# Kernel tuning notes

Measured on AMD Instinct MI355X. Metric: run time of the kernel, lower is better.

## Reference

```python
import jax, jax.numpy as jnp
import numpy as np

B, D, T = 4, 1024, 512      # z: [B, input_dim, T]
V, CD = 32000, 4096          # codebook: [codebook_size, codebook_dim]
EPS = 1e-12                  # F.normalize default eps


def setup_inputs() -> dict:
    key = jax.random.key(0)
    k1, k2, k3, k4 = jax.random.split(key, 4)
    z = jax.random.normal(k1, (B, D, T), dtype=jnp.float32)
    codebook = jax.random.normal(k2, (V, CD), dtype=jnp.float32) * 0.02
    cb_w = jax.random.normal(k3, (D, CD), dtype=jnp.float32) * 0.02  # torch Linear weight [out,in]
    cb_b = jax.random.normal(k4, (D,), dtype=jnp.float32) * 0.02
    return {"z": z, "codebook": codebook, "cb_w": cb_w, "cb_b": cb_b}


def _l2norm(x):
    n = jnp.sqrt(jnp.sum(x * x, axis=1, keepdims=True))
    return x / jnp.maximum(n, EPS)


def reference(z, codebook, cb_w, cb_b):
    # stride == 1, use_cblinear == True -> z_e = z
    z_e = z                                              # [B, D, T]
    proj_cb = codebook @ cb_w.T + cb_b                    # [V, D] cb_proj(codebook)

    # decode_latents
    enc = jnp.transpose(z_e, (0, 2, 1)).reshape(-1, D)    # (B*T, D)
    enc_n = _l2norm(enc)
    cb_n = _l2norm(proj_cb)
    dist = (jnp.sum(enc_n * enc_n, axis=1, keepdims=True)
            - 2.0 * enc_n @ cb_n.T
            + jnp.sum(cb_n * cb_n, axis=1)[None, :])      # (B*T, V)
    indices = jnp.argmax(-dist, axis=1).reshape(B, T)     # argmin distance
    z_q = jnp.transpose(proj_cb[indices], (0, 2, 1))      # gather un-normalized codes -> [B, D, T]

    commitment_loss = jnp.mean((z_e - jax.lax.stop_gradient(z_q)) ** 2, axis=(1, 2))  # [B]
    codebook_loss = jnp.mean((z_q - jax.lax.stop_gradient(z_e)) ** 2, axis=(1, 2))    # [B]
    z_q_st = z_e + jax.lax.stop_gradient(z_q - z_e)       # straight-through
    return z_q_st, indices, commitment_loss, codebook_loss
```

## Files before the change

kernel.cpp:

```cpp
#include <hip/hip_runtime.h>
#include <hip/hip_bf16.h>
#include <math.h>

#define B_  4
#define D_  1024
#define T_  512
#define V_  32000
#define CD_ 4096
#define NR  (B_*T_)
#define VT2 (V_/256)

typedef __attribute__((ext_vector_type(8))) short short8v;
typedef __attribute__((ext_vector_type(4))) float f32x4;

#define MFMA16(a,b,c) __builtin_amdgcn_mfma_f32_16x16x32_bf16((a),(b),(c),0,0,0)

#define ASM_VMCNT8() asm volatile("s_waitcnt vmcnt(8)" ::: "memory")
#define ASM_VMCNT0() asm volatile("s_waitcnt vmcnt(0)" ::: "memory")
#define ASM_LGKM0()  asm volatile("s_waitcnt lgkmcnt(0)" ::: "memory")
#define BARRIER()    do { asm volatile("" ::: "memory");            \
                          __builtin_amdgcn_s_barrier();             \
                          __builtin_amdgcn_sched_barrier(0); } while (0)

__device__ __forceinline__ unsigned short f2bf(float f) {
    return __builtin_bit_cast(unsigned short, __float2bfloat16(f));
}
__device__ __forceinline__ float bf2f(unsigned short u) {
    unsigned int v = ((unsigned int)u) << 16;
    return __builtin_bit_cast(float, v);
}
__device__ __forceinline__ void glds16(const unsigned short* g, unsigned short* l) {
    __builtin_amdgcn_global_load_lds(
        (const __attribute__((address_space(1))) unsigned int*)g,
        (__attribute__((address_space(3))) unsigned int*)l, 16, 0, 0);
}
__device__ __forceinline__ void cvt8(const float4& x, const float4& y,
                                     short8v& h, short8v& l) {
    float xs[8] = {x.x, x.y, x.z, x.w, y.x, y.y, y.z, y.w};
    #pragma unroll
    for (int e = 0; e < 8; ++e) {
        unsigned short hb = f2bf(xs[e]);
        h[e] = (short)hb;
        l[e] = (short)f2bf(xs[e] - bf2f(hb));
    }
}
__device__ __forceinline__ int xcd_swz(int wg, int nwg) {
    int q = nwg >> 3, r = nwg & 7;
    int x = wg & 7, o = wg >> 3;
    return (x < r ? x * (q + 1) : r * (q + 1) + (x - r) * q) + o;
}

__global__ __launch_bounds__(256) void vq_cvt(const float* __restrict__ x,
                                              unsigned short* __restrict__ hi,
                                              unsigned short* __restrict__ lo,
                                              size_t n4) {
    size_t stride = (size_t)gridDim.x * 256;
    for (size_t i = (size_t)blockIdx.x * 256 + threadIdx.x; i < n4; i += stride) {
        float4 v = *(const float4*)(x + 4 * i);
        float xs[4] = {v.x, v.y, v.z, v.w};
        ushort4 h, l;
        unsigned short* hp = (unsigned short*)&h;
        unsigned short* lp = (unsigned short*)&l;
        #pragma unroll
        for (int e = 0; e < 4; ++e) {
            hp[e] = f2bf(xs[e]);
            lp[e] = f2bf(xs[e] - bf2f(hp[e]));
        }
        *(ushort4*)(hi + 4 * i) = h;
        *(ushort4*)(lo + 4 * i) = l;
    }
}

#define GEMM_CORE_8P(KD)                                                      \
    f32x4 acc[8][4];                                                          \
    _Pragma("unroll")                                                         \
    for (int i = 0; i < 8; ++i)                                               \
        _Pragma("unroll")                                                     \
        for (int j = 0; j < 4; ++j) acc[i][j] = (f32x4){0.f, 0.f, 0.f, 0.f};  \
    const int lane = threadIdx.x & 63, w = threadIdx.x >> 6;                  \
    const int wr = w >> 2, wc = w & 3;                                        \
    const int r16 = lane & 15, kg = lane >> 4;                                \
    const int lane8 = lane * 8, wr8 = wr * 8, wc4 = wc * 4;                   \
    const int pw = w >> 1;                                                    \
    const unsigned short* gplane = (pw == 0) ? Ahp : (pw == 1) ? Alp          \
                                   : (pw == 2) ? Bhp : Blp;                   \
    const int baseRow = (pw < 2 ? mt : nt) + (w & 1) * 128 + r16;             \
    const unsigned short* gsrc = gplane + (size_t)baseRow * (KD) + kg * 8;    \
    unsigned short* lb0 = &smem[0][pw][(w & 1) * 4096 + lane8];               \
    unsigned short* lb1 = &smem[1][pw][(w & 1) * 4096 + lane8];               \
                                                  \
    _Pragma("unroll")                                                         \
    for (int q = 0; q < 8; ++q)                                               \
        glds16(gsrc + (size_t)q * 16 * (KD), lb0 + q * 512);                  \
    ASM_VMCNT0();                                                             \
    BARRIER();                                                                \
    const int NT = (KD) / 32;                                                 \
    for (int t = 0; t < NT; ++t) {                                            \
        const int cur = t & 1;                                                \
                      \
        if (t + 1 < NT) {                                                     \
            unsigned short* lb = cur ? lb0 : lb1;                             \
            const size_t kof = (size_t)(t + 1) * 32;                          \
            _Pragma("unroll")                                                 \
            for (int q = 0; q < 8; ++q)                                       \
                glds16(gsrc + kof + (size_t)q * 16 * (KD), lb + q * 512);     \
            ASM_VMCNT8();                                                     \
        } else {                                                              \
            ASM_VMCNT0();                                                     \
        }                                                                     \
        BARRIER();                                                            \
        short8v bh[4], bl[4];                                                 \
        _Pragma("unroll")                                                     \
        for (int nf = 0; nf < 4; ++nf) {                                      \
            bh[nf] = *(const short8v*)&smem[cur][2][(wc4 + nf) * 512 + lane8];\
            bl[nf] = *(const short8v*)&smem[cur][3][(wc4 + nf) * 512 + lane8];\
        }                                                                     \
        {                                                                     \
            short8v a0h = *(const short8v*)&smem[cur][0][(wr8 + 0) * 512 + lane8]; \
            short8v a0l = *(const short8v*)&smem[cur][1][(wr8 + 0) * 512 + lane8]; \
            short8v a1h = *(const short8v*)&smem[cur][0][(wr8 + 1) * 512 + lane8]; \
            short8v a1l = *(const short8v*)&smem[cur][1][(wr8 + 1) * 512 + lane8]; \
            __builtin_amdgcn_s_setprio(1);                                    \
            _Pragma("unroll")                                                 \
            for (int nf = 0; nf < 4; ++nf) {                                  \
                acc[0][nf] = MFMA16(a0h, bh[nf], acc[0][nf]);                 \
                acc[0][nf] = MFMA16(a0h, bl[nf], acc[0][nf]);                 \
                acc[0][nf] = MFMA16(a0l, bh[nf], acc[0][nf]);                 \
                acc[1][nf] = MFMA16(a1h, bh[nf], acc[1][nf]);                 \
                acc[1][nf] = MFMA16(a1h, bl[nf], acc[1][nf]);                 \
                acc[1][nf] = MFMA16(a1l, bh[nf], acc[1][nf]);                 \
            }                                                                 \
            __builtin_amdgcn_s_setprio(0);                                    \
        }                                                                     \
        BARRIER();                                                            \
                                                             \
        _Pragma("unroll")                                                     \
        for (int j = 1; j < 4; ++j) {                                         \
            short8v a0h = *(const short8v*)&smem[cur][0][(wr8 + 2*j) * 512 + lane8];     \
            short8v a0l = *(const short8v*)&smem[cur][1][(wr8 + 2*j) * 512 + lane8];     \
            short8v a1h = *(const short8v*)&smem[cur][0][(wr8 + 2*j + 1) * 512 + lane8]; \
            short8v a1l = *(const short8v*)&smem[cur][1][(wr8 + 2*j + 1) * 512 + lane8]; \
            BARRIER();                                                        \
            __builtin_amdgcn_s_setprio(1);                                    \
            _Pragma("unroll")                                                 \
            for (int nf = 0; nf < 4; ++nf) {                                  \
                acc[2*j][nf]   = MFMA16(a0h, bh[nf], acc[2*j][nf]);           \
                acc[2*j][nf]   = MFMA16(a0h, bl[nf], acc[2*j][nf]);           \
                acc[2*j][nf]   = MFMA16(a0l, bh[nf], acc[2*j][nf]);           \
                acc[2*j+1][nf] = MFMA16(a1h, bh[nf], acc[2*j+1][nf]);         \
                acc[2*j+1][nf] = MFMA16(a1h, bl[nf], acc[2*j+1][nf]);         \
                acc[2*j+1][nf] = MFMA16(a1l, bh[nf], acc[2*j+1][nf]);         \
            }                                                                 \
            __builtin_amdgcn_s_setprio(0);                                    \
            if (j < 3) BARRIER();                                             \
        }                                                                     \
        ASM_LGKM0();                                                          \
        BARRIER();                                                            \
    }

__global__ __launch_bounds__(512, 2) void vq_gemm1_8p(
    const unsigned short* __restrict__ Ahp, const unsigned short* __restrict__ Alp,
    const unsigned short* __restrict__ Bhp, const unsigned short* __restrict__ Blp,
    const float* __restrict__ bias,
    unsigned short* __restrict__ Phi, unsigned short* __restrict__ Plo)
{
    __shared__ unsigned short smem[2][4][8192];
    const int wg = xcd_swz(blockIdx.x, (V_/256) * (D_/256));
    const int mt = (wg >> 2) * 256;
    const int nt = (wg & 3) * 256;

    GEMM_CORE_8P(CD_)

    #pragma unroll
    for (int nf = 0; nf < 4; ++nf) {
        const int col = nt + wc * 64 + nf * 16 + r16;
        const float bv = bias[col];
        #pragma unroll
        for (int mf = 0; mf < 8; ++mf) {
            const int rbase = mt + wr * 128 + mf * 16 + kg * 4;
            #pragma unroll
            for (int r = 0; r < 4; ++r) {
                float vv = acc[mf][nf][r] + bv;
                unsigned short h = f2bf(vv);
                unsigned short l = f2bf(vv - bf2f(h));
                size_t o = (size_t)(rbase + r) * D_ + col;
                Phi[o] = h; Plo[o] = l;
            }
        }
    }
}

__global__ __launch_bounds__(512, 2) void vq_gemm2_8p(
    const unsigned short* __restrict__ Ahp, const unsigned short* __restrict__ Alp,
    const unsigned short* __restrict__ Bhp, const unsigned short* __restrict__ Blp,
    const float* __restrict__ ninv,
    float* __restrict__ pmax, int* __restrict__ pidx)
{
    __shared__ unsigned short smem[2][4][8192];
    const int wg = xcd_swz(blockIdx.x, (NR/256) * VT2);
    const int nid = wg >> 3;
    const int mt = (wg & 7) * 256;
    const int nt = nid * 256;

    GEMM_CORE_8P(D_)

    float* redv = (float*)&smem[0][0][0];
    int*   redi = (int*)&smem[0][0][2048];
    float nv[4];
    #pragma unroll
    for (int nf = 0; nf < 4; ++nf) nv[nf] = ninv[nt + wc * 64 + nf * 16 + r16];
    #pragma unroll
    for (int mf = 0; mf < 8; ++mf) {
        #pragma unroll
        for (int r = 0; r < 4; ++r) {
            float best = -INFINITY; int bi = 0x7fffffff;
            #pragma unroll
            for (int nf = 0; nf < 4; ++nf) {
                float v = acc[mf][nf][r] * nv[nf];
                int ci = nt + wc * 64 + nf * 16 + r16;
                if (v > best || (v == best && ci < bi)) { best = v; bi = ci; }
            }
            #pragma unroll
            for (int m = 8; m >= 1; m >>= 1) {
                float ov = __shfl_xor(best, m, 16);
                int   oi = __shfl_xor(bi,   m, 16);
                if (ov > best || (ov == best && oi < bi)) { best = ov; bi = oi; }
            }
            if (r16 == 0) {
                int rl = wr * 128 + mf * 16 + kg * 4 + r;
                redv[rl * 4 + wc] = best; redi[rl * 4 + wc] = bi;
            }
        }
    }
    BARRIER();
    if (threadIdx.x < 256) {
        float best = -INFINITY; int bi = 0x7fffffff;
        #pragma unroll
        for (int c = 0; c < 4; ++c) {
            float v = redv[threadIdx.x * 4 + c];
            int   i = redi[threadIdx.x * 4 + c];
            if (v > best || (v == best && i < bi)) { best = v; bi = i; }
        }
        size_t o = (size_t)(mt + threadIdx.x) * VT2 + nid;
        pmax[o] = best; pidx[o] = bi;
    }
}

__global__ __launch_bounds__(256) void vq_gemm1_mfma(
    const float* __restrict__ A,
    const unsigned short* __restrict__ Bhi, const unsigned short* __restrict__ Blo,
    const float* __restrict__ bias,
    unsigned short* __restrict__ Phi, unsigned short* __restrict__ Plo)
{
    __shared__ unsigned short smem[2][4][4096];
    const int tid = threadIdx.x;
    const int lane = tid & 63, w = tid >> 6;
    const int wr = w >> 1, wc = w & 1;
    const int m_tile = blockIdx.y * 128;
    const int n_tile = blockIdx.x * 128;
    const int row16 = lane & 15, kg = lane >> 4;
    const int s0 = 2 * w, s1 = s0 + 1;
    const int lane8 = lane * 8, wr4 = wr * 4, wc4 = wc * 4;

    const float*          Ap0 = A   + (size_t)(m_tile + s0*16 + row16) * CD_ + kg*8;
    const float*          Ap1 = A   + (size_t)(m_tile + s1*16 + row16) * CD_ + kg*8;
    const unsigned short* Bp0 = Bhi + (size_t)(n_tile + s0*16 + row16) * CD_ + kg*8;
    const unsigned short* Bp1 = Bhi + (size_t)(n_tile + s1*16 + row16) * CD_ + kg*8;
    const unsigned short* Lp0 = Blo + (size_t)(n_tile + s0*16 + row16) * CD_ + kg*8;
    const unsigned short* Lp1 = Blo + (size_t)(n_tile + s1*16 + row16) * CD_ + kg*8;

    f32x4 acc[4][4];
    #pragma unroll
    for (int i = 0; i < 4; ++i)
        #pragma unroll
        for (int j = 0; j < 4; ++j) acc[i][j] = (f32x4){0.f, 0.f, 0.f, 0.f};

    float4 aw[4], al_[4];
    aw[0] = *(const float4*)(Ap0);     aw[1] = *(const float4*)(Ap0 + 4);
    aw[2] = *(const float4*)(Ap1);     aw[3] = *(const float4*)(Ap1 + 4);
    glds16(Bp0, (unsigned short*)&smem[0][2][s0*512]);
    glds16(Bp1, (unsigned short*)&smem[0][2][s1*512]);
    glds16(Lp0, (unsigned short*)&smem[0][3][s0*512]);
    glds16(Lp1, (unsigned short*)&smem[0][3][s1*512]);
    {
        short8v h0, l0, h1, l1;
        cvt8(aw[0], aw[1], h0, l0);
        cvt8(aw[2], aw[3], h1, l1);
        *(short8v*)&smem[0][0][s0*512 + lane8] = h0;
        *(short8v*)&smem[0][1][s0*512 + lane8] = l0;
        *(short8v*)&smem[0][0][s1*512 + lane8] = h1;
        *(short8v*)&smem[0][1][s1*512 + lane8] = l1;
    }
    aw[0] = *(const float4*)(Ap0 + 32); aw[1] = *(const float4*)(Ap0 + 36);
    aw[2] = *(const float4*)(Ap1 + 32); aw[3] = *(const float4*)(Ap1 + 36);
    __syncthreads();

    int cur = 0;
    const int NT = CD_ / 32;
    for (int t = 0; t < NT; ++t) {
        if (t + 1 < NT) {
            const size_t ko = (size_t)(t + 1) * 32;
            glds16(Bp0 + ko, (unsigned short*)&smem[cur^1][2][s0*512]);
            glds16(Bp1 + ko, (unsigned short*)&smem[cur^1][2][s1*512]);
            glds16(Lp0 + ko, (unsigned short*)&smem[cur^1][3][s0*512]);
            glds16(Lp1 + ko, (unsigned short*)&smem[cur^1][3][s1*512]);
            short8v h0, l0, h1, l1;
            cvt8(aw[0], aw[1], h0, l0);
            cvt8(aw[2], aw[3], h1, l1);
            *(short8v*)&smem[cur^1][0][s0*512 + lane8] = h0;
            *(short8v*)&smem[cur^1][1][s0*512 + lane8] = l0;
            *(short8v*)&smem[cur^1][0][s1*512 + lane8] = h1;
            *(short8v*)&smem[cur^1][1][s1*512 + lane8] = l1;
        }
        if (t + 2 < NT) {
            const size_t ko2 = (size_t)(t + 2) * 32;
            al_[0] = *(const float4*)(Ap0 + ko2);  al_[1] = *(const float4*)(Ap0 + ko2 + 4);
            al_[2] = *(const float4*)(Ap1 + ko2);  al_[3] = *(const float4*)(Ap1 + ko2 + 4);
        }
        short8v ah[4], av[4], bh[4], bl[4];
        #pragma unroll
        for (int f = 0; f < 4; ++f) {
            ah[f] = *(const short8v*)&smem[cur][0][(wr4+f)*512 + lane8];
            av[f] = *(const short8v*)&smem[cur][1][(wr4+f)*512 + lane8];
            bh[f] = *(const short8v*)&smem[cur][2][(wc4+f)*512 + lane8];
            bl[f] = *(const short8v*)&smem[cur][3][(wc4+f)*512 + lane8];
        }
        #pragma unroll
        for (int mf = 0; mf < 4; ++mf)
            #pragma unroll
            for (int nf = 0; nf < 4; ++nf) {
                acc[mf][nf] = MFMA16(ah[mf], bh[nf], acc[mf][nf]);
                acc[mf][nf] = MFMA16(ah[mf], bl[nf], acc[mf][nf]);
                acc[mf][nf] = MFMA16(av[mf], bh[nf], acc[mf][nf]);
            }
        __syncthreads();
        #pragma unroll
        for (int q = 0; q < 4; ++q) aw[q] = al_[q];
        cur ^= 1;
    }

    #pragma unroll
    for (int nf = 0; nf < 4; ++nf) {
        const int col = n_tile + wc*64 + nf*16 + row16;
        const float bv = bias[col];
        #pragma unroll
        for (int mf = 0; mf < 4; ++mf) {
            const int rbase = m_tile + wr*64 + mf*16 + kg*4;
            #pragma unroll
            for (int r = 0; r < 4; ++r) {
                float vv = acc[mf][nf][r] + bv;
                unsigned short h = f2bf(vv);
                unsigned short l = f2bf(vv - bf2f(h));
                size_t o = (size_t)(rbase + r) * D_ + col;
                Phi[o] = h; Plo[o] = l;
            }
        }
    }
}

__global__ __launch_bounds__(256) void vq_norms_pl(const unsigned short* __restrict__ ph,
                                                   const unsigned short* __restrict__ pl,
                                                   float* __restrict__ ninv) {
    const int row  = blockIdx.x * 4 + (threadIdx.x >> 6);
    const int lane = threadIdx.x & 63;
    float s = 0.f;
    #pragma unroll
    for (int q = 0; q < 2; ++q) {
        size_t o = (size_t)row * D_ + q * 512 + lane * 8;
        short8v h = *(const short8v*)(ph + o);
        short8v l = *(const short8v*)(pl + o);
        #pragma unroll
        for (int e = 0; e < 8; ++e) {
            float x = bf2f((unsigned short)h[e]) + bf2f((unsigned short)l[e]);
            s += x * x;
        }
    }
    #pragma unroll
    for (int off = 32; off >= 1; off >>= 1) s += __shfl_down(s, off);
    if (lane == 0) ninv[row] = 1.0f / fmaxf(sqrtf(s), 1e-12f);
}

__global__ __launch_bounds__(256) void vq_transpose_cvt(const float* __restrict__ z,
                                                        unsigned short* __restrict__ ehi,
                                                        unsigned short* __restrict__ elo) {
    __shared__ float tile[64][65];
    const int b = blockIdx.z, t0 = blockIdx.x * 64, d0 = blockIdx.y * 64;
    const int lane = threadIdx.x & 63, sub = threadIdx.x >> 6;
    for (int dd = sub; dd < 64; dd += 4)
        tile[dd][lane] = z[((size_t)b * D_ + d0 + dd) * T_ + t0 + lane];
    __syncthreads();
    for (int tt = sub; tt < 64; tt += 4) {
        float v = tile[lane][tt];
        unsigned short h = f2bf(v);
        unsigned short l = f2bf(v - bf2f(h));
        size_t o = (size_t)(b * T_ + t0 + tt) * D_ + d0 + lane;
        ehi[o] = h; elo[o] = l;
    }
}

__global__ __launch_bounds__(256) void vq_argmerge(const float* __restrict__ pmax,
                                                   const int* __restrict__ pidx,
                                                   int* __restrict__ idxw,
                                                   float* __restrict__ outI,
                                                   int vt) {
    const int i = blockIdx.x * 256 + threadIdx.x;
    if (i >= NR) return;
    float best = -INFINITY; int bi = 0;
    for (int c = 0; c < vt; c++) {
        float v = pmax[(size_t)i * vt + c];
        int   ii = pidx[(size_t)i * vt + c];
        if (v > best || (v == best && ii < bi)) { best = v; bi = ii; }
    }
    idxw[i] = bi;
    outI[i] = (float)bi;
}

__global__ __launch_bounds__(256) void vq_gather_pl(const unsigned short* __restrict__ ph,
                                                    const unsigned short* __restrict__ pl,
                                                    const int* __restrict__ idxw,
                                                    const float* __restrict__ z,
                                                    float* __restrict__ out0,
                                                    float* __restrict__ lpart) {
    __shared__ float zq[64][65];
    __shared__ int idx_s[64];
    __shared__ float wsum[4];
    const int b = blockIdx.z, t0 = blockIdx.x * 64, d0 = blockIdx.y * 64;
    const int tid = threadIdx.x;
    const int lane = tid & 63, sub = tid >> 6;
    if (tid < 64) idx_s[tid] = idxw[b * T_ + t0 + tid];
    __syncthreads();
    for (int tt = sub; tt < 64; tt += 4) {
        size_t o = (size_t)idx_s[tt] * D_ + d0 + lane;
        zq[tt][lane] = bf2f(ph[o]) + bf2f(pl[o]);
    }
    __syncthreads();
    float lacc = 0.f;
    for (int dd = sub; dd < 64; dd += 4) {
        const size_t base = ((size_t)b * D_ + d0 + dd) * T_ + t0 + lane;
        float q = zq[lane][dd];
        float zv = z[base];
        out0[base] = q;
        float dv = zv - q;
        lacc += dv * dv;
    }
    #pragma unroll
    for (int off = 32; off >= 1; off >>= 1) lacc += __shfl_down(lacc, off);
    if (lane == 0) wsum[sub] = lacc;
    __syncthreads();
    if (tid == 0)
        lpart[(blockIdx.z * 16 + blockIdx.y) * 8 + blockIdx.x] =
            wsum[0] + wsum[1] + wsum[2] + wsum[3];
}

__global__ void vq_loss(const float* __restrict__ lpart, float* __restrict__ outL) {
    const int b = threadIdx.x;
    if (b >= B_) return;
    float s = 0.f;
    for (int q = 0; q < 128; q++) s += lpart[b * 128 + q];
    s /= (float)(D_ * T_);
    outL[b]      = s;
    outL[B_ + b] = s;
}

extern "C" void kernel_launch(void* const* d_in, const int* in_sizes, int n_in,
                              void* d_out, int out_size, void* d_ws, size_t ws_size,
                              hipStream_t stream) {
    const float* z        = (const float*)d_in[0];
    const float* codebook = (const float*)d_in[1];
    const float* cb_w     = (const float*)d_in[2];
    const float* cb_b     = (const float*)d_in[3];

    float* out0 = (float*)d_out;
    float* outI = out0 + (size_t)B_*D_*T_;
    float* outL = outI + NR;

    char* p = (char*)d_ws;
    auto alloc = [&](size_t bytes) { char* r = p; p += (bytes + 255) & ~(size_t)255; return r; };
    unsigned short* w_hi = (unsigned short*)alloc((size_t)D_ * CD_ * 2);
    unsigned short* w_lo = (unsigned short*)alloc((size_t)D_ * CD_ * 2);
    unsigned short* p_hi = (unsigned short*)alloc((size_t)V_ * D_ * 2);
    unsigned short* p_lo = (unsigned short*)alloc((size_t)V_ * D_ * 2);
    unsigned short* e_hi = (unsigned short*)alloc((size_t)NR * D_ * 2);
    unsigned short* e_lo = (unsigned short*)alloc((size_t)NR * D_ * 2);
    float* ninv  = (float*)alloc((size_t)V_ * 4);
    float* pmax  = (float*)alloc((size_t)NR * VT2 * 4);
    int*   pidx  = (int*)  alloc((size_t)NR * VT2 * 4);
    int*   idxw  = (int*)  alloc((size_t)NR * 4);
    float* lpart = (float*)alloc((size_t)2048 * 4);
    unsigned short* c_hi = (unsigned short*)alloc((size_t)V_ * CD_ * 2);
    unsigned short* c_lo = (unsigned short*)alloc((size_t)V_ * CD_ * 2);
    size_t need_full = (size_t)(p - (char*)d_ws);

    vq_cvt<<<1024, 256, 0, stream>>>(cb_w, w_hi, w_lo, (size_t)D_ * CD_ / 4);
    vq_transpose_cvt<<<dim3(T_/64, D_/64, B_), 256, 0, stream>>>(z, e_hi, e_lo);

    if (ws_size >= need_full) {
        vq_cvt<<<4096, 256, 0, stream>>>(codebook, c_hi, c_lo, (size_t)V_ * CD_ / 4);
        vq_gemm1_8p<<<(V_/256) * (D_/256), 512, 0, stream>>>(c_hi, c_lo, w_hi, w_lo,
                                                             cb_b, p_hi, p_lo);
    } else {
        vq_gemm1_mfma<<<dim3(D_/128, V_/128), 256, 0, stream>>>(codebook, w_hi, w_lo,
                                                                cb_b, p_hi, p_lo);
    }
    vq_norms_pl<<<V_/4, 256, 0, stream>>>(p_hi, p_lo, ninv);
    vq_gemm2_8p<<<(NR/256) * VT2, 512, 0, stream>>>(e_hi, e_lo, p_hi, p_lo,
                                                    ninv, pmax, pidx);
    vq_argmerge<<<NR/256, 256, 0, stream>>>(pmax, pidx, idxw, outI, VT2);
    vq_gather_pl<<<dim3(T_/64, D_/64, B_), 256, 0, stream>>>(p_hi, p_lo, idxw, z,
                                                             out0, lpart);
    vq_loss<<<1, 64, 0, stream>>>(lpart, outL);
}
```

Baseline: 1.559 ms.

## Use bf16 coarse distance GEMM with top-k candidates and exact rescoring

Measured after the change: 1.828 ms. 17.3% more time.

```diff
diff --git a/kernel.cpp b/kernel.cpp
--- a/kernel.cpp
+++ b/kernel.cpp
@@ -8,7 +8,8 @@
 #define V_  32000
 #define CD_ 4096
 #define NR  (B_*T_)
-#define VT2 (V_/256)
+#define NQ  500
+#define NCAND 16
 
 typedef __attribute__((ext_vector_type(8))) short short8v;
 typedef __attribute__((ext_vector_type(4))) float f32x4;
@@ -16,6 +17,7 @@
 #define MFMA16(a,b,c) __builtin_amdgcn_mfma_f32_16x16x32_bf16((a),(b),(c),0,0,0)
 
 #define ASM_VMCNT8() asm volatile("s_waitcnt vmcnt(8)" ::: "memory")
+#define ASM_VMCNT3() asm volatile("s_waitcnt vmcnt(3)" ::: "memory")
 #define ASM_VMCNT0() asm volatile("s_waitcnt vmcnt(0)" ::: "memory")
 #define ASM_LGKM0()  asm volatile("s_waitcnt lgkmcnt(0)" ::: "memory")
 #define BARRIER()    do { asm volatile("" ::: "memory");            \
@@ -48,6 +50,11 @@
     int q = nwg >> 3, r = nwg & 7;
     int x = wg & 7, o = wg >> 3;
     return (x < r ? x * (q + 1) : r * (q + 1) + (x - r) * q) + o;
+}
+__device__ __forceinline__ void top2_ins(float& v1, int& i1, float& v2, int& i2,
+                                         float nv, int ni) {
+    if (nv > v1 || (nv == v1 && ni < i1)) { v2 = v1; i2 = i1; v1 = nv; i1 = ni; }
+    else if (nv > v2 || (nv == v2 && ni < i2)) { v2 = nv; i2 = ni; }
 }
 
 __global__ __launch_bounds__(256) void vq_cvt(const float* __restrict__ x,
@@ -71,94 +78,7 @@
     }
 }
 
-#define GEMM_CORE_8P(KD)                                                      \
-    f32x4 acc[8][4];                                                          \
-    _Pragma("unroll")                                                         \
-    for (int i = 0; i < 8; ++i)                                               \
-        _Pragma("unroll")                                                     \
-        for (int j = 0; j < 4; ++j) acc[i][j] = (f32x4){0.f, 0.f, 0.f, 0.f};  \
-    const int lane = threadIdx.x & 63, w = threadIdx.x >> 6;                  \
-    const int wr = w >> 2, wc = w & 3;                                        \
-    const int r16 = lane & 15, kg = lane >> 4;                                \
-    const int lane8 = lane * 8, wr8 = wr * 8, wc4 = wc * 4;                   \
-    const int pw = w >> 1;                                                    \
-    const unsigned short* gplane = (pw == 0) ? Ahp : (pw == 1) ? Alp          \
-                                   : (pw == 2) ? Bhp : Blp;                   \
-    const int baseRow = (pw < 2 ? mt : nt) + (w & 1) * 128 + r16;             \
-    const unsigned short* gsrc = gplane + (size_t)baseRow * (KD) + kg * 8;    \
-    unsigned short* lb0 = &smem[0][pw][(w & 1) * 4096 + lane8];               \
-    unsigned short* lb1 = &smem[1][pw][(w & 1) * 4096 + lane8];               \
-                                                  \
-    _Pragma("unroll")                                                         \
-    for (int q = 0; q < 8; ++q)                                               \
-        glds16(gsrc + (size_t)q * 16 * (KD), lb0 + q * 512);                  \
-    ASM_VMCNT0();                                                             \
-    BARRIER();                                                                \
-    const int NT = (KD) / 32;                                                 \
-    for (int t = 0; t < NT; ++t) {                                            \
-        const int cur = t & 1;                                                \
-                      \
-        if (t + 1 < NT) {                                                     \
-            unsigned short* lb = cur ? lb0 : lb1;                             \
-            const size_t kof = (size_t)(t + 1) * 32;                          \
-            _Pragma("unroll")                                                 \
-            for (int q = 0; q < 8; ++q)                                       \
-                glds16(gsrc + kof + (size_t)q * 16 * (KD), lb + q * 512);     \
-            ASM_VMCNT8();                                                     \
-        } else {                                                              \
-            ASM_VMCNT0();                                                     \
-        }                                                                     \
-        BARRIER();                                                            \
-        short8v bh[4], bl[4];                                                 \
-        _Pragma("unroll")                                                     \
-        for (int nf = 0; nf < 4; ++nf) {                                      \
-            bh[nf] = *(const short8v*)&smem[cur][2][(wc4 + nf) * 512 + lane8];\
-            bl[nf] = *(const short8v*)&smem[cur][3][(wc4 + nf) * 512 + lane8];\
-        }                                                                     \
-        {                                                                     \
-            short8v a0h = *(const short8v*)&smem[cur][0][(wr8 + 0) * 512 + lane8]; \
-            short8v a0l = *(const short8v*)&smem[cur][1][(wr8 + 0) * 512 + lane8]; \
-            short8v a1h = *(const short8v*)&smem[cur][0][(wr8 + 1) * 512 + lane8]; \
-            short8v a1l = *(const short8v*)&smem[cur][1][(wr8 + 1) * 512 + lane8]; \
-            __builtin_amdgcn_s_setprio(1);                                    \
-            _Pragma("unroll")                                                 \
-            for (int nf = 0; nf < 4; ++nf) {                                  \
-                acc[0][nf] = MFMA16(a0h, bh[nf], acc[0][nf]);                 \
-                acc[0][nf] = MFMA16(a0h, bl[nf], acc[0][nf]);                 \
-                acc[0][nf] = MFMA16(a0l, bh[nf], acc[0][nf]);                 \
-                acc[1][nf] = MFMA16(a1h, bh[nf], acc[1][nf]);                 \
-                acc[1][nf] = MFMA16(a1h, bl[nf], acc[1][nf]);                 \
-                acc[1][nf] = MFMA16(a1l, bh[nf], acc[1][nf]);                 \
-            }                                                                 \
-            __builtin_amdgcn_s_setprio(0);                                    \
-        }                                                                     \
-        BARRIER();                                                            \
-                                                             \
-        _Pragma("unroll")                                                     \
-        for (int j = 1; j < 4; ++j) {                                         \
-            short8v a0h = *(const short8v*)&smem[cur][0][(wr8 + 2*j) * 512 + lane8];     \
-            short8v a0l = *(const short8v*)&smem[cur][1][(wr8 + 2*j) * 512 + lane8];     \
-            short8v a1h = *(const short8v*)&smem[cur][0][(wr8 + 2*j + 1) * 512 + lane8]; \
-            short8v a1l = *(const short8v*)&smem[cur][1][(wr8 + 2*j + 1) * 512 + lane8]; \
-            BARRIER();                                                        \
-            __builtin_amdgcn_s_setprio(1);                                    \
-            _Pragma("unroll")                                                 \
-            for (int nf = 0; nf < 4; ++nf) {                                  \
-                acc[2*j][nf]   = MFMA16(a0h, bh[nf], acc[2*j][nf]);           \
-                acc[2*j][nf]   = MFMA16(a0h, bl[nf], acc[2*j][nf]);           \
-                acc[2*j][nf]   = MFMA16(a0l, bh[nf], acc[2*j][nf]);           \
-                acc[2*j+1][nf] = MFMA16(a1h, bh[nf], acc[2*j+1][nf]);         \
-                acc[2*j+1][nf] = MFMA16(a1h, bl[nf], acc[2*j+1][nf]);         \
-                acc[2*j+1][nf] = MFMA16(a1l, bh[nf], acc[2*j+1][nf]);         \
-            }                                                                 \
-            __builtin_amdgcn_s_setprio(0);                                    \
-            if (j < 3) BARRIER();                                             \
-        }                                                                     \
-        ASM_LGKM0();                                                          \
-        BARRIER();                                                            \
-    }
-
-__global__ __launch_bounds__(512, 2) void vq_gemm1_8p(
+__global__ __launch_bounds__(512, 2) void vq_gemm1_v2(
     const unsigned short* __restrict__ Ahp, const unsigned short* __restrict__ Alp,
     const unsigned short* __restrict__ Bhp, const unsigned short* __restrict__ Blp,
     const float* __restrict__ bias,
@@ -168,8 +88,71 @@
     const int wg = xcd_swz(blockIdx.x, (V_/256) * (D_/256));
     const int mt = (wg >> 2) * 256;
     const int nt = (wg & 3) * 256;
-
-    GEMM_CORE_8P(CD_)
+    const int lane = threadIdx.x & 63, w = threadIdx.x >> 6;
+    const int wr = w >> 2, wc = w & 3;
+    const int r16 = lane & 15, kg = lane >> 4;
+    const int lane8 = lane * 8, wr8 = wr * 8, wc4 = wc * 4;
+    const int pw = w >> 1;
+    const unsigned short* gplane = (pw == 0) ? Ahp : (pw == 1) ? Alp
+                                   : (pw == 2) ? Bhp : Blp;
+    const int baseRow = (pw < 2 ? mt : nt) + (w & 1) * 128 + r16;
+    const unsigned short* gsrc = gplane + (size_t)baseRow * CD_ + kg * 8;
+    unsigned short* lb0 = &smem[0][pw][(w & 1) * 4096 + lane8];
+    unsigned short* lb1 = &smem[1][pw][(w & 1) * 4096 + lane8];
+
+    f32x4 acc[8][4];
+    #pragma unroll
+    for (int i = 0; i < 8; ++i)
+        #pragma unroll
+        for (int j = 0; j < 4; ++j) acc[i][j] = (f32x4){0.f, 0.f, 0.f, 0.f};
+
+    #pragma unroll
+    for (int q = 0; q < 8; ++q)
+        glds16(gsrc + (size_t)q * 16 * CD_, lb0 + q * 512);
+    ASM_VMCNT0();
+    BARRIER();
+
+    const int NT = CD_ / 32;
+    for (int t = 0; t < NT; ++t) {
+        const int cur = t & 1;
+        if (t + 1 < NT) {
+            unsigned short* lb = cur ? lb0 : lb1;
+            const size_t kof = (size_t)(t + 1) * 32;
+            #pragma unroll
+            for (int q = 0; q < 8; ++q)
+                glds16(gsrc + kof + (size_t)q * 16 * CD_, lb + q * 512);
+            ASM_VMCNT8();
+        } else {
+            ASM_VMCNT0();
+        }
+        BARRIER();
+        short8v bh[4], bl[4];
+        #pragma unroll
+        for (int nf = 0; nf < 4; ++nf) {
+            bh[nf] = *(const short8v*)&smem[cur][2][(wc4 + nf) * 512 + lane8];
+            bl[nf] = *(const short8v*)&smem[cur][3][(wc4 + nf) * 512 + lane8];
+        }
+        #pragma unroll
+        for (int g = 0; g < 4; ++g) {
+            short8v a0h = *(const short8v*)&smem[cur][0][(wr8 + 2*g) * 512 + lane8];
+            short8v a0l = *(const short8v*)&smem[cur][1][(wr8 + 2*g) * 512 + lane8];
+            short8v a1h = *(const short8v*)&smem[cur][0][(wr8 + 2*g + 1) * 512 + lane8];
+            short8v a1l = *(const short8v*)&smem[cur][1][(wr8 + 2*g + 1) * 512 + lane8];
+            __builtin_amdgcn_s_setprio(1);
+            #pragma unroll
+            for (int nf = 0; nf < 4; ++nf) {
+                acc[2*g][nf]   = MFMA16(a0h, bh[nf], acc[2*g][nf]);
+                acc[2*g][nf]   = MFMA16(a0h, bl[nf], acc[2*g][nf]);
+                acc[2*g][nf]   = MFMA16(a0l, bh[nf], acc[2*g][nf]);
+                acc[2*g+1][nf] = MFMA16(a1h, bh[nf], acc[2*g+1][nf]);
+                acc[2*g+1][nf] = MFMA16(a1h, bl[nf], acc[2*g+1][nf]);
+                acc[2*g+1][nf] = MFMA16(a1l, bh[nf], acc[2*g+1][nf]);
+            }
+            __builtin_amdgcn_s_setprio(0);
+        }
+        ASM_LGKM0();
+        BARRIER();
+    }
 
     #pragma unroll
     for (int nf = 0; nf < 4; ++nf) {
@@ -190,59 +173,186 @@
     }
 }
 
-__global__ __launch_bounds__(512, 2) void vq_gemm2_8p(
-    const unsigned short* __restrict__ Ahp, const unsigned short* __restrict__ Alp,
-    const unsigned short* __restrict__ Bhp, const unsigned short* __restrict__ Blp,
+__global__ __launch_bounds__(512, 4) void vq_gemm2_coarse(
+    const unsigned short* __restrict__ Eh, const unsigned short* __restrict__ Ph,
     const float* __restrict__ ninv,
-    float* __restrict__ pmax, int* __restrict__ pidx)
+    float* __restrict__ parrv, int* __restrict__ parri)
 {
-    __shared__ unsigned short smem[2][4][8192];
-    const int wg = xcd_swz(blockIdx.x, (NR/256) * VT2);
+    __shared__ unsigned short smE[2][8192];
+    __shared__ unsigned short smP[2][4096];
+    const int wg = xcd_swz(blockIdx.x, 8 * (V_/128));
     const int nid = wg >> 3;
     const int mt = (wg & 7) * 256;
-    const int nt = nid * 256;
-
-    GEMM_CORE_8P(D_)
-
-    float* redv = (float*)&smem[0][0][0];
-    int*   redi = (int*)&smem[0][0][2048];
+    const int nt = nid * 128;
+    const int lane = threadIdx.x & 63, w = threadIdx.x >> 6;
+    const int wr = w >> 1, wc = w & 1;
+    const int r16 = lane & 15, kg = lane >> 4;
+    const int lane8 = lane * 8, wr4 = wr * 4, wc4 = wc * 4;
+
+    const unsigned short* gsrcu[3];
+    unsigned short* l0[3];
+    unsigned short* l1[3];
+    #pragma unroll
+    for (int q = 0; q < 3; ++q) {
+        int u = w * 3 + q;
+        int isP = (u >= 16);
+        int sub = isP ? u - 16 : u;
+        int row = (isP ? nt : mt) + sub * 16 + r16;
+        gsrcu[q] = (isP ? Ph : Eh) + (size_t)row * D_ + kg * 8;
+        l0[q] = isP ? &smP[0][sub*512 + lane8] : &smE[0][sub*512 + lane8];
+        l1[q] = isP ? &smP[1][sub*512 + lane8] : &smE[1][sub*512 + lane8];
+    }
+
+    f32x4 acc[4][4];
+    #pragma unroll
+    for (int i = 0; i < 4; ++i)
+        #pragma unroll
+        for (int j = 0; j < 4; ++j) acc[i][j] = (f32x4){0.f, 0.f, 0.f, 0.f};
+
+    #pragma unroll
+    for (int q = 0; q < 3; ++q) glds16(gsrcu[q], l0[q]);
+    ASM_VMCNT0();
+    BARRIER();
+
+    const int NT = D_ / 32;
+    for (int t = 0; t < NT; ++t) {
+        const int cur = t & 1;
+        if (t + 1 < NT) {
+            const size_t kof = (size_t)(t + 1) * 32;
+            #pragma unroll
+            for (int q = 0; q < 3; ++q)
+                glds16(gsrcu[q] + kof, cur ? l0[q] : l1[q]);
+            ASM_VMCNT3();
+        } else {
+            ASM_VMCNT0();
+        }
+        BARRIER();
+        short8v bfr[4], afr[4];
+        #pragma unroll
+        for (int nf = 0; nf < 4; ++nf)
+            bfr[nf] = *(const short8v*)&smP[cur][(wc4 + nf) * 512 + lane8];
+        #pragma unroll
+        for (int mf = 0; mf < 4; ++mf)
+            afr[mf] = *(const short8v*)&smE[cur][(wr4 + mf) * 512 + lane8];
+        __builtin_amdgcn_s_setprio(1);
+        #pragma unroll
+        for (int mf = 0; mf < 4; ++mf)
+            #pragma unroll
+            for (int nf = 0; nf < 4; ++nf)
+                acc[mf][nf] = MFMA16(afr[mf], bfr[nf], acc[mf][nf]);
+        __builtin_amdgcn_s_setprio(0);
+        ASM_LGKM0();
+        BARRIER();
+    }
+
+    const int qid = nid * 2 + wc;
     float nv[4];
     #pragma unroll
     for (int nf = 0; nf < 4; ++nf) nv[nf] = ninv[nt + wc * 64 + nf * 16 + r16];
     #pragma unroll
-    for (int mf = 0; mf < 8; ++mf) {
+    for (int mf = 0; mf < 4; ++mf) {
         #pragma unroll
         for (int r = 0; r < 4; ++r) {
-            float best = -INFINITY; int bi = 0x7fffffff;
+            float v1 = -INFINITY, v2 = -INFINITY;
+            int i1 = 0x7fffffff, i2 = 0x7fffffff;
             #pragma unroll
             for (int nf = 0; nf < 4; ++nf) {
-                float v = acc[mf][nf][r] * nv[nf];
+                float s = acc[mf][nf][r] * nv[nf];
                 int ci = nt + wc * 64 + nf * 16 + r16;
-                if (v > best || (v == best && ci < bi)) { best = v; bi = ci; }
+                top2_ins(v1, i1, v2, i2, s, ci);
             }
             #pragma unroll
             for (int m = 8; m >= 1; m >>= 1) {
-                float ov = __shfl_xor(best, m, 16);
-                int   oi = __shfl_xor(bi,   m, 16);
-                if (ov > best || (ov == best && oi < bi)) { best = ov; bi = oi; }
+                float ov1 = __shfl_xor(v1, m, 16); int oi1 = __shfl_xor(i1, m, 16);
+                float ov2 = __shfl_xor(v2, m, 16); int oi2 = __shfl_xor(i2, m, 16);
+                top2_ins(v1, i1, v2, i2, ov1, oi1);
+                top2_ins(v1, i1, v2, i2, ov2, oi2);
             }
             if (r16 == 0) {
-                int rl = wr * 128 + mf * 16 + kg * 4 + r;
-                redv[rl * 4 + wc] = best; redi[rl * 4 + wc] = bi;
+                const int row = mt + wr * 64 + mf * 16 + kg * 4 + r;
+                size_t off = (size_t)row * (NQ * 2) + qid * 2;
+                parrv[off] = v1;     parri[off] = i1;
+                parrv[off + 1] = v2; parri[off + 1] = i2;
             }
         }
     }
-    BARRIER();
-    if (threadIdx.x < 256) {
-        float best = -INFINITY; int bi = 0x7fffffff;
-        #pragma unroll
-        for (int c = 0; c < 4; ++c) {
-            float v = redv[threadIdx.x * 4 + c];
-            int   i = redi[threadIdx.x * 4 + c];
-            if (v > best || (v == best && i < bi)) { best = v; bi = i; }
-        }
-        size_t o = (size_t)(mt + threadIdx.x) * VT2 + nid;
-        pmax[o] = best; pidx[o] = bi;
+}
+
+__global__ __launch_bounds__(256) void vq_top16(const float* __restrict__ parrv,
+                                                const int* __restrict__ parri,
+                                                int* __restrict__ cand) {
+    const int row = blockIdx.x * 4 + (threadIdx.x >> 6);
+    const int lane = threadIdx.x & 63;
+    float v[16]; int id[16];
+    #pragma unroll
+    for (int q = 0; q < 16; ++q) {
+        int s = lane + q * 64;
+        if (s < NQ * 2) {
+            v[q] = parrv[(size_t)row * (NQ * 2) + s];
+            id[q] = parri[(size_t)row * (NQ * 2) + s];
+        } else { v[q] = -INFINITY; id[q] = 0x7fffffff; }
+    }
+    for (int k = 0; k < NCAND; ++k) {
+        float bv = -INFINITY; int bi = 0x7fffffff;
+        #pragma unroll
+        for (int q = 0; q < 16; ++q)
+            if (v[q] > bv || (v[q] == bv && id[q] < bi)) { bv = v[q]; bi = id[q]; }
+        #pragma unroll
+        for (int m = 32; m >= 1; m >>= 1) {
+            float ov = __shfl_xor(bv, m, 64); int oi = __shfl_xor(bi, m, 64);
+            if (ov > bv || (ov == bv && oi < bi)) { bv = ov; bi = oi; }
+        }
+        cand[row * NCAND + k] = bi;
+        #pragma unroll
+        for (int q = 0; q < 16; ++q)
+            if (id[q] == bi) v[q] = -INFINITY;
+    }
+}
+
+__global__ __launch_bounds__(256) void vq_rescore(
+    const unsigned short* __restrict__ eh, const unsigned short* __restrict__ el,
+    const unsigned short* __restrict__ ph, const unsigned short* __restrict__ pl,
+    const float* __restrict__ ninv, const int* __restrict__ cand,
+    int* __restrict__ idxw, float* __restrict__ outI) {
+    __shared__ float e[D_];
+    __shared__ double wsum[NCAND][4];
+    const int row = blockIdx.x;
+    const int tid = threadIdx.x, lane = tid & 63, wv = tid >> 6;
+    {
+        ushort4 h = *(const ushort4*)(eh + (size_t)row * D_ + tid * 4);
+        ushort4 l = *(const ushort4*)(el + (size_t)row * D_ + tid * 4);
+        const unsigned short* hp = (const unsigned short*)&h;
+        const unsigned short* lp = (const unsigned short*)&l;
+        #pragma unroll
+        for (int j = 0; j < 4; ++j)
+            e[tid * 4 + j] = bf2f(hp[j]) + bf2f(lp[j]);
+    }
+    __syncthreads();
+    for (int c = 0; c < NCAND; ++c) {
+        int cv = cand[row * NCAND + c];
+        ushort4 h = *(const ushort4*)(ph + (size_t)cv * D_ + tid * 4);
+        ushort4 l = *(const ushort4*)(pl + (size_t)cv * D_ + tid * 4);
+        const unsigned short* hp = (const unsigned short*)&h;
+        const unsigned short* lp = (const unsigned short*)&l;
+        double s = 0.0;
+        #pragma unroll
+        for (int j = 0; j < 4; ++j)
+            s += (double)e[tid * 4 + j] * (double)(bf2f(hp[j]) + bf2f(lp[j]));
+        #pragma unroll
+        for (int off = 32; off >= 1; off >>= 1) s += __shfl_down(s, off);
+        if (lane == 0) wsum[c][wv] = s;
+    }
+    __syncthreads();
+    if (tid == 0) {
+        double best = -1.0e300; int bi = 0x7fffffff;
+        for (int c = 0; c < NCAND; ++c) {
+            int cv = cand[row * NCAND + c];
+            double s = (wsum[c][0] + wsum[c][1] + wsum[c][2] + wsum[c][3])
+                       * (double)ninv[cv];
+            if (s > best || (s == best && cv < bi)) { best = s; bi = cv; }
+        }
+        idxw[row] = bi;
+        outI[row] = (float)bi;
     }
 }
 
@@ -396,23 +506,6 @@
         size_t o = (size_t)(b * T_ + t0 + tt) * D_ + d0 + lane;
         ehi[o] = h; elo[o] = l;
     }
-}
-
-__global__ __launch_bounds__(256) void vq_argmerge(const float* __restrict__ pmax,
-                                                   const int* __restrict__ pidx,
-                                                   int* __restrict__ idxw,
-                                                   float* __restrict__ outI,
-                                                   int vt) {
-    const int i = blockIdx.x * 256 + threadIdx.x;
-    if (i >= NR) return;
-    float best = -INFINITY; int bi = 0;
-    for (int c = 0; c < vt; c++) {
-        float v = pmax[(size_t)i * vt + c];
-        int   ii = pidx[(size_t)i * vt + c];
-        if (v > best || (v == best && ii < bi)) { best = v; bi = ii; }
-    }
-    idxw[i] = bi;
-    outI[i] = (float)bi;
 }
 
 __global__ __launch_bounds__(256) void vq_gather_pl(const unsigned short* __restrict__ ph,
@@ -483,8 +576,9 @@
     unsigned short* e_hi = (unsigned short*)alloc((size_t)NR * D_ * 2);
     unsigned short* e_lo = (unsigned short*)alloc((size_t)NR * D_ * 2);
     float* ninv  = (float*)alloc((size_t)V_ * 4);
-    float* pmax  = (float*)alloc((size_t)NR * VT2 * 4);
-    int*   pidx  = (int*)  alloc((size_t)NR * VT2 * 4);
+    float* parrv = (float*)alloc((size_t)NR * NQ * 2 * 4);
+    int*   parri = (int*)  alloc((size_t)NR * NQ * 2 * 4);
+    int*   cand  = (int*)  alloc((size_t)NR * NCAND * 4);
     int*   idxw  = (int*)  alloc((size_t)NR * 4);
     float* lpart = (float*)alloc((size_t)2048 * 4);
     unsigned short* c_hi = (unsigned short*)alloc((size_t)V_ * CD_ * 2);
@@ -496,16 +590,16 @@
 
     if (ws_size >= need_full) {
         vq_cvt<<<4096, 256, 0, stream>>>(codebook, c_hi, c_lo, (size_t)V_ * CD_ / 4);
-        vq_gemm1_8p<<<(V_/256) * (D_/256), 512, 0, stream>>>(c_hi, c_lo, w_hi, w_lo,
+        vq_gemm1_v2<<<(V_/256) * (D_/256), 512, 0, stream>>>(c_hi, c_lo, w_hi, w_lo,
                                                              cb_b, p_hi, p_lo);
     } else {
         vq_gemm1_mfma<<<dim3(D_/128, V_/128), 256, 0, stream>>>(codebook, w_hi, w_lo,
                                                                 cb_b, p_hi, p_lo);
     }
     vq_norms_pl<<<V_/4, 256, 0, stream>>>(p_hi, p_lo, ninv);
-    vq_gemm2_8p<<<(NR/256) * VT2, 512, 0, stream>>>(e_hi, e_lo, p_hi, p_lo,
-                                                    ninv, pmax, pidx);
-    vq_argmerge<<<NR/256, 256, 0, stream>>>(pmax, pidx, idxw, outI, VT2);
+    vq_gemm2_coarse<<<8 * (V_/128), 512, 0, stream>>>(e_hi, p_hi, ninv, parrv, parri);
+    vq_top16<<<NR/4, 256, 0, stream>>>(parrv, parri, cand);
+    vq_rescore<<<NR, 256, 0, stream>>>(e_hi, e_lo, p_hi, p_lo, ninv, cand, idxw, outI);
     vq_gather_pl<<<dim3(T_/64, D_/64, B_), 256, 0, stream>>>(p_hi, p_lo, idxw, z,
                                                              out0, lpart);
     vq_loss<<<1, 64, 0, stream>>>(lpart, outL);
```

## Restructure split-bf16 GEMM main loop into four barrier-synchronized phases with deferred prefetch wait

Applied to the files above, without the earlier changes.

Result: no change. 1.546 ms (-0.8%).

```diff
diff --git a/kernel.cpp b/kernel.cpp
--- a/kernel.cpp
+++ b/kernel.cpp
@@ -15,12 +15,9 @@
 
 #define MFMA16(a,b,c) __builtin_amdgcn_mfma_f32_16x16x32_bf16((a),(b),(c),0,0,0)
 
-#define ASM_VMCNT8() asm volatile("s_waitcnt vmcnt(8)" ::: "memory")
 #define ASM_VMCNT0() asm volatile("s_waitcnt vmcnt(0)" ::: "memory")
 #define ASM_LGKM0()  asm volatile("s_waitcnt lgkmcnt(0)" ::: "memory")
-#define BARRIER()    do { asm volatile("" ::: "memory");            \
-                          __builtin_amdgcn_s_barrier();             \
-                          __builtin_amdgcn_sched_barrier(0); } while (0)
+#define SCHED_BAR()  __builtin_amdgcn_sched_barrier(0)
 
 __device__ __forceinline__ unsigned short f2bf(float f) {
     return __builtin_bit_cast(unsigned short, __float2bfloat16(f));
@@ -71,7 +68,33 @@
     }
 }
 
-#define GEMM_CORE_8P(KD)                                                      \
+#define T8_PHASE(pp, EXTRA)                                                   \
+    {                                                                         \
+        short8v aAh = *(const short8v*)&smem[cur][0][(wr8 + 2*(pp)) * 512 + lane8];     \
+        short8v aAl = *(const short8v*)&smem[cur][1][(wr8 + 2*(pp)) * 512 + lane8];     \
+        short8v aBh = *(const short8v*)&smem[cur][0][(wr8 + 2*(pp) + 1) * 512 + lane8]; \
+        short8v aBl = *(const short8v*)&smem[cur][1][(wr8 + 2*(pp) + 1) * 512 + lane8]; \
+        EXTRA;                                                                \
+        SCHED_BAR();                                                          \
+        __builtin_amdgcn_s_barrier();                                         \
+        ASM_LGKM0();                                                          \
+        SCHED_BAR();                                                          \
+        __builtin_amdgcn_s_setprio(1);                                        \
+        _Pragma("unroll")                                                     \
+        for (int nf = 0; nf < 4; ++nf) {                                      \
+            acc[2*(pp)][nf]   = MFMA16(aAh, bh[nf], acc[2*(pp)][nf]);         \
+            acc[2*(pp)][nf]   = MFMA16(aAh, bl[nf], acc[2*(pp)][nf]);         \
+            acc[2*(pp)][nf]   = MFMA16(aAl, bh[nf], acc[2*(pp)][nf]);         \
+            acc[2*(pp)+1][nf] = MFMA16(aBh, bh[nf], acc[2*(pp)+1][nf]);       \
+            acc[2*(pp)+1][nf] = MFMA16(aBh, bl[nf], acc[2*(pp)+1][nf]);       \
+            acc[2*(pp)+1][nf] = MFMA16(aBl, bh[nf], acc[2*(pp)+1][nf]);       \
+        }                                                                     \
+        __builtin_amdgcn_s_setprio(0);                                        \
+        __builtin_amdgcn_s_barrier();                                         \
+        SCHED_BAR();                                                          \
+    }
+
+#define T8_CORE(KD)                                                           \
     f32x4 acc[8][4];                                                          \
     _Pragma("unroll")                                                         \
     for (int i = 0; i < 8; ++i)                                               \
@@ -88,77 +111,35 @@
     const unsigned short* gsrc = gplane + (size_t)baseRow * (KD) + kg * 8;    \
     unsigned short* lb0 = &smem[0][pw][(w & 1) * 4096 + lane8];               \
     unsigned short* lb1 = &smem[1][pw][(w & 1) * 4096 + lane8];               \
-                                                  \
     _Pragma("unroll")                                                         \
     for (int q = 0; q < 8; ++q)                                               \
         glds16(gsrc + (size_t)q * 16 * (KD), lb0 + q * 512);                  \
     ASM_VMCNT0();                                                             \
-    BARRIER();                                                                \
+    __builtin_amdgcn_s_barrier();                                             \
+    SCHED_BAR();                                                              \
     const int NT = (KD) / 32;                                                 \
     for (int t = 0; t < NT; ++t) {                                            \
         const int cur = t & 1;                                                \
-                      \
-        if (t + 1 < NT) {                                                     \
-            unsigned short* lb = cur ? lb0 : lb1;                             \
-            const size_t kof = (size_t)(t + 1) * 32;                          \
-            _Pragma("unroll")                                                 \
-            for (int q = 0; q < 8; ++q)                                       \
-                glds16(gsrc + kof + (size_t)q * 16 * (KD), lb + q * 512);     \
-            ASM_VMCNT8();                                                     \
-        } else {                                                              \
-            ASM_VMCNT0();                                                     \
-        }                                                                     \
-        BARRIER();                                                            \
+        unsigned short* lbN = cur ? lb0 : lb1;                                \
         short8v bh[4], bl[4];                                                 \
         _Pragma("unroll")                                                     \
         for (int nf = 0; nf < 4; ++nf) {                                      \
             bh[nf] = *(const short8v*)&smem[cur][2][(wc4 + nf) * 512 + lane8];\
             bl[nf] = *(const short8v*)&smem[cur][3][(wc4 + nf) * 512 + lane8];\
         }                                                                     \
-        {                                                                     \
-            short8v a0h = *(const short8v*)&smem[cur][0][(wr8 + 0) * 512 + lane8]; \
-            short8v a0l = *(const short8v*)&smem[cur][1][(wr8 + 0) * 512 + lane8]; \
-            short8v a1h = *(const short8v*)&smem[cur][0][(wr8 + 1) * 512 + lane8]; \
-            short8v a1l = *(const short8v*)&smem[cur][1][(wr8 + 1) * 512 + lane8]; \
-            __builtin_amdgcn_s_setprio(1);                                    \
-            _Pragma("unroll")                                                 \
-            for (int nf = 0; nf < 4; ++nf) {                                  \
-                acc[0][nf] = MFMA16(a0h, bh[nf], acc[0][nf]);                 \
-                acc[0][nf] = MFMA16(a0h, bl[nf], acc[0][nf]);                 \
-                acc[0][nf] = MFMA16(a0l, bh[nf], acc[0][nf]);                 \
-                acc[1][nf] = MFMA16(a1h, bh[nf], acc[1][nf]);                 \
-                acc[1][nf] = MFMA16(a1h, bl[nf], acc[1][nf]);                 \
-                acc[1][nf] = MFMA16(a1l, bh[nf], acc[1][nf]);                 \
-            }                                                                 \
-            __builtin_amdgcn_s_setprio(0);                                    \
-        }                                                                     \
-        BARRIER();                                                            \
-                                                             \
-        _Pragma("unroll")                                                     \
-        for (int j = 1; j < 4; ++j) {                                         \
-            short8v a0h = *(const short8v*)&smem[cur][0][(wr8 + 2*j) * 512 + lane8];     \
-            short8v a0l = *(const short8v*)&smem[cur][1][(wr8 + 2*j) * 512 + lane8];     \
-            short8v a1h = *(const short8v*)&smem[cur][0][(wr8 + 2*j + 1) * 512 + lane8]; \
-            short8v a1l = *(const short8v*)&smem[cur][1][(wr8 + 2*j + 1) * 512 + lane8]; \
-            BARRIER();                                                        \
-            __builtin_amdgcn_s_setprio(1);                                    \
-            _Pragma("unroll")                                                 \
-            for (int nf = 0; nf < 4; ++nf) {                                  \
-                acc[2*j][nf]   = MFMA16(a0h, bh[nf], acc[2*j][nf]);           \
-                acc[2*j][nf]   = MFMA16(a0h, bl[nf], acc[2*j][nf]);           \
-                acc[2*j][nf]   = MFMA16(a0l, bh[nf], acc[2*j][nf]);           \
-                acc[2*j+1][nf] = MFMA16(a1h, bh[nf], acc[2*j+1][nf]);         \
-                acc[2*j+1][nf] = MFMA16(a1h, bl[nf], acc[2*j+1][nf]);         \
-                acc[2*j+1][nf] = MFMA16(a1l, bh[nf], acc[2*j+1][nf]);         \
-            }                                                                 \
-            __builtin_amdgcn_s_setprio(0);                                    \
-            if (j < 3) BARRIER();                                             \
-        }                                                                     \
-        ASM_LGKM0();                                                          \
-        BARRIER();                                                            \
-    }
-
-__global__ __launch_bounds__(512, 2) void vq_gemm1_8p(
+        T8_PHASE(0,                                                           \
+            if (t + 1 < NT) {                                                 \
+                const size_t kof = (size_t)(t + 1) * 32;                      \
+                _Pragma("unroll")                                             \
+                for (int q = 0; q < 8; ++q)                                   \
+                    glds16(gsrc + kof + (size_t)q * 16 * (KD), lbN + q * 512);\
+            })                                                                \
+        T8_PHASE(1, (void)0)                                                  \
+        T8_PHASE(2, (void)0)                                                  \
+        T8_PHASE(3, if (t + 1 < NT) { ASM_VMCNT0(); })                        \
+    }
+
+__global__ __launch_bounds__(512, 2) void vq_gemm1_t8(
     const unsigned short* __restrict__ Ahp, const unsigned short* __restrict__ Alp,
     const unsigned short* __restrict__ Bhp, const unsigned short* __restrict__ Blp,
     const float* __restrict__ bias,
@@ -169,7 +150,7 @@
     const int mt = (wg >> 2) * 256;
     const int nt = (wg & 3) * 256;
 
-    GEMM_CORE_8P(CD_)
+    T8_CORE(CD_)
 
     #pragma unroll
     for (int nf = 0; nf < 4; ++nf) {
@@ -190,7 +171,7 @@
     }
 }
 
-__global__ __launch_bounds__(512, 2) void vq_gemm2_8p(
+__global__ __launch_bounds__(512, 2) void vq_gemm2_t8(
     const unsigned short* __restrict__ Ahp, const unsigned short* __restrict__ Alp,
     const unsigned short* __restrict__ Bhp, const unsigned short* __restrict__ Blp,
     const float* __restrict__ ninv,
@@ -202,7 +183,7 @@
     const int mt = (wg & 7) * 256;
     const int nt = nid * 256;
 
-    GEMM_CORE_8P(D_)
+    T8_CORE(D_)
 
     float* redv = (float*)&smem[0][0][0];
     int*   redi = (int*)&smem[0][0][2048];
@@ -232,7 +213,7 @@
             }
         }
     }
-    BARRIER();
+    __builtin_amdgcn_s_barrier();
     if (threadIdx.x < 256) {
         float best = -INFINITY; int bi = 0x7fffffff;
         #pragma unroll
@@ -496,14 +477,14 @@
 
     if (ws_size >= need_full) {
         vq_cvt<<<4096, 256, 0, stream>>>(codebook, c_hi, c_lo, (size_t)V_ * CD_ / 4);
-        vq_gemm1_8p<<<(V_/256) * (D_/256), 512, 0, stream>>>(c_hi, c_lo, w_hi, w_lo,
+        vq_gemm1_t8<<<(V_/256) * (D_/256), 512, 0, stream>>>(c_hi, c_lo, w_hi, w_lo,
                                                              cb_b, p_hi, p_lo);
     } else {
         vq_gemm1_mfma<<<dim3(D_/128, V_/128), 256, 0, stream>>>(codebook, w_hi, w_lo,
                                                                 cb_b, p_hi, p_lo);
     }
     vq_norms_pl<<<V_/4, 256, 0, stream>>>(p_hi, p_lo, ninv);
-    vq_gemm2_8p<<<(NR/256) * VT2, 512, 0, stream>>>(e_hi, e_lo, p_hi, p_lo,
+    vq_gemm2_t8<<<(NR/256) * VT2, 512, 0, stream>>>(e_hi, e_lo, p_hi, p_lo,
                                                     ninv, pmax, pidx);
     vq_argmerge<<<NR/256, 256, 0, stream>>>(pmax, pidx, idxw, outI, VT2);
     vq_gather_pl<<<dim3(T_/64, D_/64, B_), 256, 0, stream>>>(p_hi, p_lo, idxw, z,
```
